# Optimization experiments

Hardware: AMD Instinct MI355X
Metric: run time of the kernel (lower is better)

Reference implementation:

```python
import jax, jax.numpy as jnp
import numpy as np

S, R, C, H, D = 128, 384, 256, 8, 32  # N_seq, N_res, C_m, heads, head_dim
INF = 1e9
EPS = 1e-5


def _layernorm(x, w, b):
    mu = jnp.mean(x, axis=-1, keepdims=True)
    var = jnp.mean(jnp.square(x - mu), axis=-1, keepdims=True)
    return (x - mu) * jax.lax.rsqrt(var + EPS) * w + b


def setup_inputs() -> dict:
    key = jax.random.key(0)
    ks = jax.random.split(key, 8)
    sc = 0.02
    m = jax.random.normal(ks[0], (S, R, C), jnp.float32)
    mask = jnp.ones((S, R), jnp.float32)
    ln_w = jnp.ones((C,), jnp.float32)
    ln_b = jnp.zeros((C,), jnp.float32)
    wq = jax.random.normal(ks[1], (C, H * D), jnp.float32) * sc
    wk = jax.random.normal(ks[2], (C, H * D), jnp.float32) * sc
    wv = jax.random.normal(ks[3], (C, H * D), jnp.float32) * sc
    wg = jax.random.normal(ks[4], (C, H * D), jnp.float32) * sc
    bg = jnp.ones((H * D,), jnp.float32)  # gate bias init to 1 (openfold convention)
    wo = jax.random.normal(ks[5], (H * D, C), jnp.float32) * sc
    bo = jnp.zeros((C,), jnp.float32)
    return {"m": m, "mask": mask, "ln_w": ln_w, "ln_b": ln_b,
            "wq": wq, "wk": wk, "wv": wv, "wg": wg, "bg": bg,
            "wo": wo, "bo": bo}


def reference(m, mask, ln_w, ln_b, wq, wk, wv, wg, bg, wo, bo):
    # mask bias: [S, 1, 1, R], 0 where mask==1, -inf-ish where mask==0
    mask_bias = (INF * (mask - 1.0))[:, None, None, :]
    x = _layernorm(m, ln_w, ln_b)                        # [S, R, C]
    q = (x @ wq).reshape(S, R, H, D) * (D ** -0.5)       # [S, R, H, D]
    k = (x @ wk).reshape(S, R, H, D)
    v = (x @ wv).reshape(S, R, H, D)
    scores = jnp.einsum('sqhd,skhd->shqk', q, k) + mask_bias  # [S, H, R, R]
    a = jax.nn.softmax(scores, axis=-1)
    o = jnp.einsum('shqk,skhd->sqhd', a, v)              # [S, R, H, D]
    g = jax.nn.sigmoid(x @ wg + bg).reshape(S, R, H, D)  # gate
    o = (o * g).reshape(S, R, H * D)
    return o @ wo + bo                                   # [S, R, C]
```

## Files before the change

### kernel.cpp

```cpp
#include <hip/hip_runtime.h>
#include <cstdint>
#include <cstddef>

#define S_  128
#define R_  384
#define C_  256
#define H_  8
#define D_  32
#define HD_ 256
#define M_  (S_*R_)

#define LOG2E 1.4426950408889634f

typedef float f32x16 __attribute__((ext_vector_type(16)));
typedef short s16x8  __attribute__((ext_vector_type(8)));
typedef int   i32x4  __attribute__((ext_vector_type(4)));

__device__ __forceinline__ unsigned short f2bf(float f) {
  uint32_t u = __float_as_uint(f);
  u += 0x7fffu + ((u >> 16) & 1u);
  return (unsigned short)(u >> 16);
}
__device__ __forceinline__ float bf2f(unsigned short s) {
  return __uint_as_float(((uint32_t)s) << 16);
}
__device__ __forceinline__ uint32_t pkbf(float lo, float hi) {
  return (uint32_t)f2bf(lo) | ((uint32_t)f2bf(hi) << 16);
}
#define MFMA32(a,b,c) __builtin_amdgcn_mfma_f32_32x32x16_bf16((a),(b),(c),0,0,0)

__device__ __forceinline__ void gload16(const void* g, void* l) {
  __builtin_amdgcn_global_load_lds(
      (const __attribute__((address_space(1))) void*)g,
      (__attribute__((address_space(3))) void*)l, 16, 0, 0);
}

__global__ __launch_bounds__(256) void prep_w(const float* __restrict__ wq,
    const float* __restrict__ wk, const float* __restrict__ wv,
    const float* __restrict__ wg, const float* __restrict__ wo,
    unsigned short* __restrict__ WT) {
  __shared__ unsigned short Tl[64][72];
  const int mat = blockIdx.x >> 4;
  const int t   = blockIdx.x & 15;
  const int k0  = (t >> 2) * 64, n0 = (t & 3) * 64;
  const float* W = (mat==0)?wq:(mat==1)?wk:(mat==2)?wv:(mat==3)?wg:wo;
  const int tx = threadIdx.x & 63, ty = threadIdx.x >> 6;
#pragma unroll
  for (int i = 0; i < 16; i++) {
    int kk = ty + i * 4;
    Tl[tx][kk] = f2bf(W[(size_t)(k0 + kk) * 256 + n0 + tx]);
  }
  __syncthreads();
#pragma unroll
  for (int i = 0; i < 16; i++) {
    int nn = ty + i * 4;
    WT[(size_t)mat * 65536 + (size_t)(n0 + nn) * 256 + k0 + tx] = Tl[nn][tx];
  }
}

__global__ __launch_bounds__(256) void ln_kernel(const float* __restrict__ mIn,
    const float* __restrict__ w, const float* __restrict__ b,
    unsigned short* __restrict__ x) {
  int row  = blockIdx.x * 4 + (threadIdx.x >> 6);
  int lane = threadIdx.x & 63;
  const float4 v4 = *(const float4*)(mIn + (size_t)row * C_ + lane * 4);
  float s  = v4.x + v4.y + v4.z + v4.w;
  float ss = v4.x*v4.x + v4.y*v4.y + v4.z*v4.z + v4.w*v4.w;
#pragma unroll
  for (int off = 32; off > 0; off >>= 1) {
    s  += __shfl_xor(s,  off);
    ss += __shfl_xor(ss, off);
  }
  float mu  = s * (1.0f / C_);
  float var = ss * (1.0f / C_) - mu * mu;
  float rs  = rsqrtf(var + 1e-5f);
  const float4 wv = *(const float4*)(w + lane * 4);
  const float4 bv = *(const float4*)(b + lane * 4);
  uint2 o2;
  o2.x = pkbf((v4.x - mu) * rs * wv.x + bv.x, (v4.y - mu) * rs * wv.y + bv.y);
  o2.y = pkbf((v4.z - mu) * rs * wv.z + bv.z, (v4.w - mu) * rs * wv.w + bv.w);
  *(uint2*)(x + (size_t)row * C_ + lane * 4) = o2;
}

__global__ __launch_bounds__(256) void proj_gemm(const unsigned short* __restrict__ X,
    const unsigned short* __restrict__ WT, const float* __restrict__ bg,
    unsigned short* __restrict__ Qo, unsigned short* __restrict__ Ko,
    unsigned short* __restrict__ Vo, unsigned short* __restrict__ Go) {
  __shared__ __align__(16) unsigned short As[128 * 32];
  __shared__ __align__(16) unsigned short Bs[128 * 32];
  const int tid = threadIdx.x;
  const int bm  = blockIdx.x * 128;
  const int wi  = blockIdx.y >> 1;
  const int bn  = (blockIdx.y & 1) * 128;
  const unsigned short* Wt = WT + (size_t)wi * 65536;
  unsigned short* O = (wi==0)?Qo:(wi==1)?Ko:(wi==2)?Vo:Go;

  const int lane = tid & 63, wid = tid >> 6;
  const int wm = (wid >> 1) * 64, wn = (wid & 1) * 64;
  const int lr = lane & 31, hi = lane >> 5;
  const int srow = lane >> 2, scol = (lane & 3) * 8;

  f32x16 acc[2][2];
#pragma unroll
  for (int i = 0; i < 2; i++)
#pragma unroll
    for (int j = 0; j < 2; j++)
#pragma unroll
      for (int r = 0; r < 16; r++) acc[i][j][r] = 0.f;

  for (int k0 = 0; k0 < 256; k0 += 32) {
#pragma unroll
    for (int i = 0; i < 2; i++) {
      const int rbase = wid * 32 + i * 16;
      gload16(X  + (size_t)(bm + rbase + srow) * 256 + k0 + scol, &As[rbase * 32]);
      gload16(Wt + (size_t)(bn + rbase + srow) * 256 + k0 + scol, &Bs[rbase * 32]);
    }
    asm volatile("s_waitcnt vmcnt(0)" ::: "memory");
    __syncthreads();
#pragma unroll
    for (int kh = 0; kh < 2; kh++) {
      s16x8 a0 = *(const s16x8*)&As[(wm + lr) * 32      + kh*16 + 8*hi];
      s16x8 a1 = *(const s16x8*)&As[(wm + 32 + lr) * 32 + kh*16 + 8*hi];
      s16x8 b0 = *(const s16x8*)&Bs[(wn + lr) * 32      + kh*16 + 8*hi];
      s16x8 b1 = *(const s16x8*)&Bs[(wn + 32 + lr) * 32 + kh*16 + 8*hi];
      acc[0][0] = MFMA32(a0, b0, acc[0][0]);
      acc[0][1] = MFMA32(a0, b1, acc[0][1]);
      acc[1][0] = MFMA32(a1, b0, acc[1][0]);
      acc[1][1] = MFMA32(a1, b1, acc[1][1]);
    }
    __syncthreads();
  }

  const float qs2 = 0.17677669529663687f * LOG2E;
#pragma unroll
  for (int ms = 0; ms < 2; ms++) {
#pragma unroll
    for (int ns = 0; ns < 2; ns++) {
      int colg = bn + wn + ns*32 + lr;
      float bgv = (wi == 3) ? bg[colg] : 0.f;
#pragma unroll
      for (int r = 0; r < 16; r++) {
        float v = acc[ms][ns][r];
        if (wi == 0) v *= qs2;
        if (wi == 3) v = 1.0f / (1.0f + __expf(-(v + bgv)));
        int row = bm + wm + ms*32 + (r & 3) + 8*(r >> 2) + 4*hi;
        O[(size_t)row * 256 + colg] = f2bf(v);
      }
    }
  }
}

__global__ __launch_bounds__(256) void attn_kernel(const unsigned short* __restrict__ Qb,
    const unsigned short* __restrict__ Kb, const unsigned short* __restrict__ Vb,
    const unsigned short* __restrict__ Gb, const float* __restrict__ mask,
    unsigned short* __restrict__ Ob) {
  __shared__ unsigned short Kl[192][40];
  __shared__ unsigned short VT[32][200];
  __shared__ float mb[384];
  __shared__ float sAl[4][32];

  const int h = blockIdx.x, s = blockIdx.y;
  const int tid = threadIdx.x;
  const int wid = tid >> 6;
  const int lane = tid & 63;
  const int lr = lane & 31, hi = lane >> 5;

  for (int r = tid; r < 384; r += 256)
    mb[r] = (1e9f * LOG2E) * (mask[s * R_ + r] - 1.0f);

  s16x8 bq[3][2];
#pragma unroll
  for (int st = 0; st < 3; st++)
#pragma unroll
    for (int kh = 0; kh < 2; kh++)
      bq[st][kh] = *(const s16x8*)(Qb + ((size_t)(s*R_ + wid*96 + st*32 + lr)) * 256
                                   + h*32 + kh*16 + 8*hi);

  f32x16 of[3];
#pragma unroll
  for (int st = 0; st < 3; st++)
#pragma unroll
    for (int r = 0; r < 16; r++) of[st][r] = 0.f;
  float mrun[3] = {-1e30f, -1e30f, -1e30f};
  float lsum[3] = {0.f, 0.f, 0.f};

  for (int ph = 0; ph < 2; ph++) {
    __syncthreads();
#pragma unroll
    for (int i = 0; i < 2; i++) {
      int rh = tid + 256 * i;
      if (rh < 384) {
        int rl = rh >> 1, c0 = (rh & 1) * 16;
        int rg = ph * 192 + rl;
        const unsigned short* ksrc = Kb + ((size_t)(s*R_ + rg)) * 256 + h*32 + c0;
        *(uint4*)&Kl[rl][c0]     = *(const uint4*)ksrc;
        *(uint4*)&Kl[rl][c0 + 8] = *(const uint4*)(ksrc + 8);
        const unsigned short* vsrc = Vb + ((size_t)(s*R_ + rg)) * 256 + h*32 + c0;
        unsigned short tmp[16];
        *(uint4*)tmp       = *(const uint4*)vsrc;
        *(uint4*)(tmp + 8) = *(const uint4*)(vsrc + 8);
#pragma unroll
        for (int j = 0; j < 16; j++) VT[c0 + j][rl] = tmp[j];
      }
    }
    __syncthreads();

    for (int kt = 0; kt < 6; kt++) {
      const int ktg = ph * 6 + kt;
      s16x8 ak0 = *(const s16x8*)&Kl[kt*32 + lr][8*hi];
      s16x8 ak1 = *(const s16x8*)&Kl[kt*32 + lr][16 + 8*hi];
      s16x8 bv0 = *(const s16x8*)&VT[lr][kt*32 + 8*hi];
      s16x8 bv1 = *(const s16x8*)&VT[lr][kt*32 + 16 + 8*hi];
      float mbr[16];
#pragma unroll
      for (int r = 0; r < 16; r++) mbr[r] = mb[ktg*32 + (r & 3) + 8*(r >> 2) + 4*hi];

#pragma unroll
      for (int st = 0; st < 3; st++) {
        f32x16 p;
#pragma unroll
        for (int r = 0; r < 16; r++) p[r] = mbr[r];
        __builtin_amdgcn_s_setprio(1);
        p = MFMA32(ak0, bq[st][0], p);
        p = MFMA32(ak1, bq[st][1], p);
        __builtin_amdgcn_s_setprio(0);
        float m01 = fmaxf(fmaxf(p[0], p[1]), fmaxf(p[2], p[3]));
        float m23 = fmaxf(fmaxf(p[4], p[5]), fmaxf(p[6], p[7]));
        float m45 = fmaxf(fmaxf(p[8], p[9]), fmaxf(p[10], p[11]));
        float m67 = fmaxf(fmaxf(p[12], p[13]), fmaxf(p[14], p[15]));
        float pm = fmaxf(fmaxf(m01, m23), fmaxf(m45, m67));
        pm = fmaxf(pm, __shfl_xor(pm, 32));
        if (!__all(pm <= mrun[st] + 11.54f)) {
          float nm = fmaxf(mrun[st], pm);
          float al = __builtin_amdgcn_exp2f(mrun[st] - nm);
          mrun[st] = nm;
          lsum[st] *= al;
          if (hi == 0) sAl[wid][lr] = al;
          float alr[16];
#pragma unroll
          for (int r = 0; r < 16; r++) alr[r] = sAl[wid][(r & 3) + 8*(r >> 2) + 4*hi];
#pragma unroll
          for (int r = 0; r < 16; r++) of[st][r] *= alr[r];
        }
        float ls = 0.f;
#pragma unroll
        for (int r = 0; r < 16; r++) {
          p[r] = __builtin_amdgcn_exp2f(p[r] - mrun[st]);
          ls += p[r];
        }
        lsum[st] += ls;
        uint32_t w0 = pkbf(p[0],  p[1]),  w1 = pkbf(p[2],  p[3]);
        uint32_t w2 = pkbf(p[4],  p[5]),  w3 = pkbf(p[6],  p[7]);
        uint32_t w4 = pkbf(p[8],  p[9]),  w5 = pkbf(p[10], p[11]);
        uint32_t w6 = pkbf(p[12], p[13]), w7 = pkbf(p[14], p[15]);
        asm volatile("v_permlane32_swap_b32 %0, %1" : "+v"(w0), "+v"(w2));
        asm volatile("v_permlane32_swap_b32 %0, %1" : "+v"(w1), "+v"(w3));
        asm volatile("v_permlane32_swap_b32 %0, %1" : "+v"(w4), "+v"(w6));
        asm volatile("v_permlane32_swap_b32 %0, %1" : "+v"(w5), "+v"(w7));
        i32x4 pa0i = {(int)w0, (int)w1, (int)w2, (int)w3};
        i32x4 pa1i = {(int)w4, (int)w5, (int)w6, (int)w7};
        __builtin_amdgcn_s_setprio(1);
        of[st] = MFMA32(__builtin_bit_cast(s16x8, pa0i), bv0, of[st]);
        of[st] = MFMA32(__builtin_bit_cast(s16x8, pa1i), bv1, of[st]);
        __builtin_amdgcn_s_setprio(0);
      }
    }
  }

#pragma unroll
  for (int st = 0; st < 3; st++) {
    float lt = lsum[st] + __shfl_xor(lsum[st], 32);
    float inv = 1.0f / lt;
    if (hi == 0) sAl[wid][lr] = inv;
    float ivr[16];
#pragma unroll
    for (int r = 0; r < 16; r++) ivr[r] = sAl[wid][(r & 3) + 8*(r >> 2) + 4*hi];
#pragma unroll
    for (int r = 0; r < 16; r++) {
      int row = wid*96 + st*32 + (r & 3) + 8*(r >> 2) + 4*hi;
      size_t off = ((size_t)(s*R_ + row)) * 256 + h*32 + lr;
      float gv = bf2f(Gb[off]);
      Ob[off] = f2bf(of[st][r] * ivr[r] * gv);
    }
  }
}

__global__ __launch_bounds__(256) void out_gemm(const unsigned short* __restrict__ Ob,
    const unsigned short* __restrict__ WT, const float* __restrict__ bo,
    float* __restrict__ Out) {
  __shared__ __align__(16) unsigned short As[128 * 32];
  __shared__ __align__(16) unsigned short Bs[128 * 32];
  const unsigned short* Wt = WT + 4 * 65536;
  const int tid = threadIdx.x;
  const int bm = blockIdx.x * 128;
  const int bn = blockIdx.y * 128;
  const int lane = tid & 63, wid = tid >> 6;
  const int wm = (wid >> 1) * 64, wn = (wid & 1) * 64;
  const int lr = lane & 31, hi = lane >> 5;
  const int srow = lane >> 2, scol = (lane & 3) * 8;

  f32x16 acc[2][2];
#pragma unroll
  for (int i = 0; i < 2; i++)
#pragma unroll
    for (int j = 0; j < 2; j++)
#pragma unroll
      for (int r = 0; r < 16; r++) acc[i][j][r] = 0.f;

  for (int k0 = 0; k0 < 256; k0 += 32) {
#pragma unroll
    for (int i = 0; i < 2; i++) {
      const int rbase = wid * 32 + i * 16;
      gload16(Ob + (size_t)(bm + rbase + srow) * 256 + k0 + scol, &As[rbase * 32]);
      gload16(Wt + (size_t)(bn + rbase + srow) * 256 + k0 + scol, &Bs[rbase * 32]);
    }
    asm volatile("s_waitcnt vmcnt(0)" ::: "memory");
    __syncthreads();
#pragma unroll
    for (int kh = 0; kh < 2; kh++) {
      s16x8 a0 = *(const s16x8*)&As[(wm + lr) * 32      + kh*16 + 8*hi];
      s16x8 a1 = *(const s16x8*)&As[(wm + 32 + lr) * 32 + kh*16 + 8*hi];
      s16x8 b0 = *(const s16x8*)&Bs[(wn + lr) * 32      + kh*16 + 8*hi];
      s16x8 b1 = *(const s16x8*)&Bs[(wn + 32 + lr) * 32 + kh*16 + 8*hi];
      acc[0][0] = MFMA32(a0, b0, acc[0][0]);
      acc[0][1] = MFMA32(a0, b1, acc[0][1]);
      acc[1][0] = MFMA32(a1, b0, acc[1][0]);
      acc[1][1] = MFMA32(a1, b1, acc[1][1]);
    }
    __syncthreads();
  }

#pragma unroll
  for (int ms = 0; ms < 2; ms++) {
#pragma unroll
    for (int ns = 0; ns < 2; ns++) {
      int colg = bn + wn + ns*32 + lr;
      float bov = bo[colg];
#pragma unroll
      for (int r = 0; r < 16; r++) {
        int row = bm + wm + ms*32 + (r & 3) + 8*(r >> 2) + 4*hi;
        Out[(size_t)row * 256 + colg] = acc[ms][ns][r] + bov;
      }
    }
  }
}

extern "C" void kernel_launch(void* const* d_in, const int* in_sizes, int n_in,
                              void* d_out, int out_size, void* d_ws, size_t ws_size,
                              hipStream_t stream) {
  const float* m    = (const float*)d_in[0];
  const float* mask = (const float*)d_in[1];
  const float* ln_w = (const float*)d_in[2];
  const float* ln_b = (const float*)d_in[3];
  const float* wq   = (const float*)d_in[4];
  const float* wk   = (const float*)d_in[5];
  const float* wv   = (const float*)d_in[6];
  const float* wg   = (const float*)d_in[7];
  const float* bg   = (const float*)d_in[8];
  const float* wo   = (const float*)d_in[9];
  const float* bo   = (const float*)d_in[10];
  float* out = (float*)d_out;

  unsigned short* ws = (unsigned short*)d_ws;
  const size_t SZ = (size_t)M_ * 256;
  unsigned short* xbf = ws;
  unsigned short* qb  = ws + 1 * SZ;
  unsigned short* kb  = ws + 2 * SZ;
  unsigned short* vb  = ws + 3 * SZ;
  unsigned short* gb  = ws + 4 * SZ;
  unsigned short* ob  = ws + 5 * SZ;
  unsigned short* WT  = ws + 6 * SZ;

  prep_w<<<80, 256, 0, stream>>>(wq, wk, wv, wg, wo, WT);
  ln_kernel<<<M_ / 4, 256, 0, stream>>>(m, ln_w, ln_b, xbf);
  proj_gemm<<<dim3(M_ / 128, 8), 256, 0, stream>>>(xbf, WT, bg, qb, kb, vb, gb);
  attn_kernel<<<dim3(H_, S_), 256, 0, stream>>>(qb, kb, vb, gb, mask, ob);
  out_gemm<<<dim3(M_ / 128, 2), 256, 0, stream>>>(ob, WT, bo, out);
}
```

Measured before the change: 262.3 us.

## Shrink GEMM tiles, reorder grids, and use 12-wave attention blocks

```diff
diff --git a/kernel.cpp b/kernel.cpp
--- a/kernel.cpp
+++ b/kernel.cpp
@@ -82,265 +82,233 @@
   *(uint2*)(x + (size_t)row * C_ + lane * 4) = o2;
 }
 
-__global__ __launch_bounds__(256) void proj_gemm(const unsigned short* __restrict__ X,
+__global__ __launch_bounds__(256, 5) void proj_gemm(const unsigned short* __restrict__ X,
     const unsigned short* __restrict__ WT, const float* __restrict__ bg,
     unsigned short* __restrict__ Qo, unsigned short* __restrict__ Ko,
     unsigned short* __restrict__ Vo, unsigned short* __restrict__ Go) {
-  __shared__ __align__(16) unsigned short As[128 * 32];
+  __shared__ __align__(16) unsigned short As[64 * 32];
   __shared__ __align__(16) unsigned short Bs[128 * 32];
   const int tid = threadIdx.x;
-  const int bm  = blockIdx.x * 128;
-  const int wi  = blockIdx.y >> 1;
-  const int bn  = (blockIdx.y & 1) * 128;
+  const int wi  = blockIdx.x >> 1;
+  const int bn  = (blockIdx.x & 1) * 128;
+  const int bm  = blockIdx.y * 64;
   const unsigned short* Wt = WT + (size_t)wi * 65536;
   unsigned short* O = (wi==0)?Qo:(wi==1)?Ko:(wi==2)?Vo:Go;
 
   const int lane = tid & 63, wid = tid >> 6;
-  const int wm = (wid >> 1) * 64, wn = (wid & 1) * 64;
+  const int wr = (wid >> 1) * 32, wc = (wid & 1) * 64;
   const int lr = lane & 31, hi = lane >> 5;
   const int srow = lane >> 2, scol = (lane & 3) * 8;
 
-  f32x16 acc[2][2];
-#pragma unroll
-  for (int i = 0; i < 2; i++)
-#pragma unroll
-    for (int j = 0; j < 2; j++)
-#pragma unroll
-      for (int r = 0; r < 16; r++) acc[i][j][r] = 0.f;
+  f32x16 acc0, acc1;
+#pragma unroll
+  for (int r = 0; r < 16; r++) { acc0[r] = 0.f; acc1[r] = 0.f; }
 
   for (int k0 = 0; k0 < 256; k0 += 32) {
+    gload16(X + (size_t)(bm + wid*16 + srow) * 256 + k0 + scol, &As[wid * 512]);
 #pragma unroll
     for (int i = 0; i < 2; i++) {
-      const int rbase = wid * 32 + i * 16;
-      gload16(X  + (size_t)(bm + rbase + srow) * 256 + k0 + scol, &As[rbase * 32]);
-      gload16(Wt + (size_t)(bn + rbase + srow) * 256 + k0 + scol, &Bs[rbase * 32]);
+      const int rb = wid * 32 + i * 16;
+      gload16(Wt + (size_t)(bn + rb + srow) * 256 + k0 + scol, &Bs[rb * 32]);
     }
     asm volatile("s_waitcnt vmcnt(0)" ::: "memory");
     __syncthreads();
 #pragma unroll
     for (int kh = 0; kh < 2; kh++) {
-      s16x8 a0 = *(const s16x8*)&As[(wm + lr) * 32      + kh*16 + 8*hi];
-      s16x8 a1 = *(const s16x8*)&As[(wm + 32 + lr) * 32 + kh*16 + 8*hi];
-      s16x8 b0 = *(const s16x8*)&Bs[(wn + lr) * 32      + kh*16 + 8*hi];
-      s16x8 b1 = *(const s16x8*)&Bs[(wn + 32 + lr) * 32 + kh*16 + 8*hi];
-      acc[0][0] = MFMA32(a0, b0, acc[0][0]);
-      acc[0][1] = MFMA32(a0, b1, acc[0][1]);
-      acc[1][0] = MFMA32(a1, b0, acc[1][0]);
-      acc[1][1] = MFMA32(a1, b1, acc[1][1]);
+      s16x8 a0 = *(const s16x8*)&As[(wr + lr) * 32      + kh*16 + 8*hi];
+      s16x8 b0 = *(const s16x8*)&Bs[(wc + lr) * 32      + kh*16 + 8*hi];
+      s16x8 b1 = *(const s16x8*)&Bs[(wc + 32 + lr) * 32 + kh*16 + 8*hi];
+      acc0 = MFMA32(a0, b0, acc0);
+      acc1 = MFMA32(a0, b1, acc1);
     }
     __syncthreads();
   }
 
   const float qs2 = 0.17677669529663687f * LOG2E;
 #pragma unroll
-  for (int ms = 0; ms < 2; ms++) {
-#pragma unroll
-    for (int ns = 0; ns < 2; ns++) {
-      int colg = bn + wn + ns*32 + lr;
-      float bgv = (wi == 3) ? bg[colg] : 0.f;
-#pragma unroll
-      for (int r = 0; r < 16; r++) {
-        float v = acc[ms][ns][r];
-        if (wi == 0) v *= qs2;
-        if (wi == 3) v = 1.0f / (1.0f + __expf(-(v + bgv)));
-        int row = bm + wm + ms*32 + (r & 3) + 8*(r >> 2) + 4*hi;
-        O[(size_t)row * 256 + colg] = f2bf(v);
-      }
-    }
-  }
-}
-
-__global__ __launch_bounds__(256) void attn_kernel(const unsigned short* __restrict__ Qb,
+  for (int ns = 0; ns < 2; ns++) {
+    const f32x16& a = ns ? acc1 : acc0;
+    int colg = bn + wc + ns*32 + lr;
+    float bgv = (wi == 3) ? bg[colg] : 0.f;
+#pragma unroll
+    for (int r = 0; r < 16; r++) {
+      float v = a[r];
+      if (wi == 0) v *= qs2;
+      if (wi == 3) v = 1.0f / (1.0f + __expf(-(v + bgv)));
+      int row = bm + wr + (r & 3) + 8*(r >> 2) + 4*hi;
+      O[(size_t)row * 256 + colg] = f2bf(v);
+    }
+  }
+}
+
+__global__ __launch_bounds__(768, 6) void attn_kernel(const unsigned short* __restrict__ Qb,
     const unsigned short* __restrict__ Kb, const unsigned short* __restrict__ Vb,
     const unsigned short* __restrict__ Gb, const float* __restrict__ mask,
     unsigned short* __restrict__ Ob) {
-  __shared__ unsigned short Kl[192][40];
-  __shared__ unsigned short VT[32][200];
+  __shared__ unsigned short Kl[384][40];
+  __shared__ unsigned short VT[32][392];
   __shared__ float mb[384];
-  __shared__ float sAl[4][32];
+  __shared__ float sAl[12][32];
 
   const int h = blockIdx.x, s = blockIdx.y;
   const int tid = threadIdx.x;
-  const int wid = tid >> 6;
-  const int lane = tid & 63;
+  const int wid = tid >> 6, lane = tid & 63;
   const int lr = lane & 31, hi = lane >> 5;
 
-  for (int r = tid; r < 384; r += 256)
-    mb[r] = (1e9f * LOG2E) * (mask[s * R_ + r] - 1.0f);
-
-  s16x8 bq[3][2];
-#pragma unroll
-  for (int st = 0; st < 3; st++)
-#pragma unroll
-    for (int kh = 0; kh < 2; kh++)
-      bq[st][kh] = *(const s16x8*)(Qb + ((size_t)(s*R_ + wid*96 + st*32 + lr)) * 256
-                                   + h*32 + kh*16 + 8*hi);
-
-  f32x16 of[3];
-#pragma unroll
-  for (int st = 0; st < 3; st++)
-#pragma unroll
-    for (int r = 0; r < 16; r++) of[st][r] = 0.f;
-  float mrun[3] = {-1e30f, -1e30f, -1e30f};
-  float lsum[3] = {0.f, 0.f, 0.f};
-
-  for (int ph = 0; ph < 2; ph++) {
-    __syncthreads();
-#pragma unroll
-    for (int i = 0; i < 2; i++) {
-      int rh = tid + 256 * i;
-      if (rh < 384) {
-        int rl = rh >> 1, c0 = (rh & 1) * 16;
-        int rg = ph * 192 + rl;
-        const unsigned short* ksrc = Kb + ((size_t)(s*R_ + rg)) * 256 + h*32 + c0;
-        *(uint4*)&Kl[rl][c0]     = *(const uint4*)ksrc;
-        *(uint4*)&Kl[rl][c0 + 8] = *(const uint4*)(ksrc + 8);
-        const unsigned short* vsrc = Vb + ((size_t)(s*R_ + rg)) * 256 + h*32 + c0;
-        unsigned short tmp[16];
-        *(uint4*)tmp       = *(const uint4*)vsrc;
-        *(uint4*)(tmp + 8) = *(const uint4*)(vsrc + 8);
-#pragma unroll
-        for (int j = 0; j < 16; j++) VT[c0 + j][rl] = tmp[j];
-      }
-    }
-    __syncthreads();
-
-    for (int kt = 0; kt < 6; kt++) {
-      const int ktg = ph * 6 + kt;
-      s16x8 ak0 = *(const s16x8*)&Kl[kt*32 + lr][8*hi];
-      s16x8 ak1 = *(const s16x8*)&Kl[kt*32 + lr][16 + 8*hi];
-      s16x8 bv0 = *(const s16x8*)&VT[lr][kt*32 + 8*hi];
-      s16x8 bv1 = *(const s16x8*)&VT[lr][kt*32 + 16 + 8*hi];
-      float mbr[16];
-#pragma unroll
-      for (int r = 0; r < 16; r++) mbr[r] = mb[ktg*32 + (r & 3) + 8*(r >> 2) + 4*hi];
-
-#pragma unroll
-      for (int st = 0; st < 3; st++) {
-        f32x16 p;
-#pragma unroll
-        for (int r = 0; r < 16; r++) p[r] = mbr[r];
-        __builtin_amdgcn_s_setprio(1);
-        p = MFMA32(ak0, bq[st][0], p);
-        p = MFMA32(ak1, bq[st][1], p);
-        __builtin_amdgcn_s_setprio(0);
-        float m01 = fmaxf(fmaxf(p[0], p[1]), fmaxf(p[2], p[3]));
-        float m23 = fmaxf(fmaxf(p[4], p[5]), fmaxf(p[6], p[7]));
-        float m45 = fmaxf(fmaxf(p[8], p[9]), fmaxf(p[10], p[11]));
-        float m67 = fmaxf(fmaxf(p[12], p[13]), fmaxf(p[14], p[15]));
-        float pm = fmaxf(fmaxf(m01, m23), fmaxf(m45, m67));
-        pm = fmaxf(pm, __shfl_xor(pm, 32));
-        if (!__all(pm <= mrun[st] + 11.54f)) {
-          float nm = fmaxf(mrun[st], pm);
-          float al = __builtin_amdgcn_exp2f(mrun[st] - nm);
-          mrun[st] = nm;
-          lsum[st] *= al;
-          if (hi == 0) sAl[wid][lr] = al;
-          float alr[16];
-#pragma unroll
-          for (int r = 0; r < 16; r++) alr[r] = sAl[wid][(r & 3) + 8*(r >> 2) + 4*hi];
-#pragma unroll
-          for (int r = 0; r < 16; r++) of[st][r] *= alr[r];
-        }
-        float ls = 0.f;
-#pragma unroll
-        for (int r = 0; r < 16; r++) {
-          p[r] = __builtin_amdgcn_exp2f(p[r] - mrun[st]);
-          ls += p[r];
-        }
-        lsum[st] += ls;
-        uint32_t w0 = pkbf(p[0],  p[1]),  w1 = pkbf(p[2],  p[3]);
-        uint32_t w2 = pkbf(p[4],  p[5]),  w3 = pkbf(p[6],  p[7]);
-        uint32_t w4 = pkbf(p[8],  p[9]),  w5 = pkbf(p[10], p[11]);
-        uint32_t w6 = pkbf(p[12], p[13]), w7 = pkbf(p[14], p[15]);
-        asm volatile("v_permlane32_swap_b32 %0, %1" : "+v"(w0), "+v"(w2));
-        asm volatile("v_permlane32_swap_b32 %0, %1" : "+v"(w1), "+v"(w3));
-        asm volatile("v_permlane32_swap_b32 %0, %1" : "+v"(w4), "+v"(w6));
-        asm volatile("v_permlane32_swap_b32 %0, %1" : "+v"(w5), "+v"(w7));
-        i32x4 pa0i = {(int)w0, (int)w1, (int)w2, (int)w3};
-        i32x4 pa1i = {(int)w4, (int)w5, (int)w6, (int)w7};
-        __builtin_amdgcn_s_setprio(1);
-        of[st] = MFMA32(__builtin_bit_cast(s16x8, pa0i), bv0, of[st]);
-        of[st] = MFMA32(__builtin_bit_cast(s16x8, pa1i), bv1, of[st]);
-        __builtin_amdgcn_s_setprio(0);
-      }
-    }
-  }
-
-#pragma unroll
-  for (int st = 0; st < 3; st++) {
-    float lt = lsum[st] + __shfl_xor(lsum[st], 32);
-    float inv = 1.0f / lt;
-    if (hi == 0) sAl[wid][lr] = inv;
-    float ivr[16];
-#pragma unroll
-    for (int r = 0; r < 16; r++) ivr[r] = sAl[wid][(r & 3) + 8*(r >> 2) + 4*hi];
+  if (tid < 384) {
+    const unsigned short* ksrc = Kb + ((size_t)(s*R_ + tid)) * 256 + h*32;
+    uint4 k0 = *(const uint4*)ksrc;
+    uint4 k1 = *(const uint4*)(ksrc + 8);
+    uint4 k2 = *(const uint4*)(ksrc + 16);
+    uint4 k3 = *(const uint4*)(ksrc + 24);
+    *(uint4*)&Kl[tid][0]  = k0;
+    *(uint4*)&Kl[tid][8]  = k1;
+    *(uint4*)&Kl[tid][16] = k2;
+    *(uint4*)&Kl[tid][24] = k3;
+    mb[tid] = (1e9f * LOG2E) * (mask[s * R_ + tid] - 1.0f);
+  } else {
+    const int r = tid - 384;
+    const unsigned short* vsrc = Vb + ((size_t)(s*R_ + r)) * 256 + h*32;
+    unsigned short tmp[32];
+    *(uint4*)(tmp)      = *(const uint4*)vsrc;
+    *(uint4*)(tmp + 8)  = *(const uint4*)(vsrc + 8);
+    *(uint4*)(tmp + 16) = *(const uint4*)(vsrc + 16);
+    *(uint4*)(tmp + 24) = *(const uint4*)(vsrc + 24);
+#pragma unroll
+    for (int j = 0; j < 32; j++) VT[j][r] = tmp[j];
+  }
+
+  const int q0 = wid * 32;
+  const unsigned short* qsrc = Qb + ((size_t)(s*R_ + q0 + lr)) * 256 + h*32;
+  s16x8 bq0 = *(const s16x8*)(qsrc + 8*hi);
+  s16x8 bq1 = *(const s16x8*)(qsrc + 16 + 8*hi);
+
+  f32x16 of;
+#pragma unroll
+  for (int r = 0; r < 16; r++) of[r] = 0.f;
+  float mrun = -1e30f, lsum = 0.f;
+
+  __syncthreads();
+
+  for (int kt = 0; kt < 12; kt++) {
+    s16x8 ak0 = *(const s16x8*)&Kl[kt*32 + lr][8*hi];
+    s16x8 ak1 = *(const s16x8*)&Kl[kt*32 + lr][16 + 8*hi];
+    s16x8 bv0 = *(const s16x8*)&VT[lr][kt*32 + 8*hi];
+    s16x8 bv1 = *(const s16x8*)&VT[lr][kt*32 + 16 + 8*hi];
+
+    f32x16 p;
+#pragma unroll
+    for (int r = 0; r < 16; r++) p[r] = mb[kt*32 + (r & 3) + 8*(r >> 2) + 4*hi];
+    __builtin_amdgcn_s_setprio(1);
+    p = MFMA32(ak0, bq0, p);
+    p = MFMA32(ak1, bq1, p);
+    __builtin_amdgcn_s_setprio(0);
+
+    float m01 = fmaxf(fmaxf(p[0], p[1]), fmaxf(p[2], p[3]));
+    float m23 = fmaxf(fmaxf(p[4], p[5]), fmaxf(p[6], p[7]));
+    float m45 = fmaxf(fmaxf(p[8], p[9]), fmaxf(p[10], p[11]));
+    float m67 = fmaxf(fmaxf(p[12], p[13]), fmaxf(p[14], p[15]));
+    float pm = fmaxf(fmaxf(m01, m23), fmaxf(m45, m67));
+    pm = fmaxf(pm, __shfl_xor(pm, 32));
+    if (!__all(pm <= mrun + 11.54f)) {
+      float nm = fmaxf(mrun, pm);
+      float al = __builtin_amdgcn_exp2f(mrun - nm);
+      mrun = nm;
+      lsum *= al;
+      if (hi == 0) sAl[wid][lr] = al;
+#pragma unroll
+      for (int r = 0; r < 16; r++)
+        of[r] *= sAl[wid][(r & 3) + 8*(r >> 2) + 4*hi];
+    }
+    float ls = 0.f;
 #pragma unroll
     for (int r = 0; r < 16; r++) {
-      int row = wid*96 + st*32 + (r & 3) + 8*(r >> 2) + 4*hi;
-      size_t off = ((size_t)(s*R_ + row)) * 256 + h*32 + lr;
-      float gv = bf2f(Gb[off]);
-      Ob[off] = f2bf(of[st][r] * ivr[r] * gv);
-    }
-  }
-}
-
-__global__ __launch_bounds__(256) void out_gemm(const unsigned short* __restrict__ Ob,
+      p[r] = __builtin_amdgcn_exp2f(p[r] - mrun);
+      ls += p[r];
+    }
+    lsum += ls;
+
+    uint32_t w0, w1, w2, w3, w4, w5, w6, w7;
+    asm("v_cvt_pk_bf16_f32 %0, %1, %2" : "=v"(w0) : "v"(p[0]),  "v"(p[1]));
+    asm("v_cvt_pk_bf16_f32 %0, %1, %2" : "=v"(w1) : "v"(p[2]),  "v"(p[3]));
+    asm("v_cvt_pk_bf16_f32 %0, %1, %2" : "=v"(w2) : "v"(p[4]),  "v"(p[5]));
+    asm("v_cvt_pk_bf16_f32 %0, %1, %2" : "=v"(w3) : "v"(p[6]),  "v"(p[7]));
+    asm("v_cvt_pk_bf16_f32 %0, %1, %2" : "=v"(w4) : "v"(p[8]),  "v"(p[9]));
+    asm("v_cvt_pk_bf16_f32 %0, %1, %2" : "=v"(w5) : "v"(p[10]), "v"(p[11]));
+    asm("v_cvt_pk_bf16_f32 %0, %1, %2" : "=v"(w6) : "v"(p[12]), "v"(p[13]));
+    asm("v_cvt_pk_bf16_f32 %0, %1, %2" : "=v"(w7) : "v"(p[14]), "v"(p[15]));
+    asm volatile("v_permlane32_swap_b32 %0, %1" : "+v"(w0), "+v"(w2));
+    asm volatile("v_permlane32_swap_b32 %0, %1" : "+v"(w1), "+v"(w3));
+    asm volatile("v_permlane32_swap_b32 %0, %1" : "+v"(w4), "+v"(w6));
+    asm volatile("v_permlane32_swap_b32 %0, %1" : "+v"(w5), "+v"(w7));
+    i32x4 pa0i = {(int)w0, (int)w1, (int)w2, (int)w3};
+    i32x4 pa1i = {(int)w4, (int)w5, (int)w6, (int)w7};
+    __builtin_amdgcn_s_setprio(1);
+    of = MFMA32(__builtin_bit_cast(s16x8, pa0i), bv0, of);
+    of = MFMA32(__builtin_bit_cast(s16x8, pa1i), bv1, of);
+    __builtin_amdgcn_s_setprio(0);
+  }
+
+  float lt = lsum + __shfl_xor(lsum, 32);
+  float inv = 1.0f / lt;
+  if (hi == 0) sAl[wid][lr] = inv;
+#pragma unroll
+  for (int r = 0; r < 16; r++) {
+    int crow = (r & 3) + 8*(r >> 2) + 4*hi;
+    float iv = sAl[wid][crow];
+    size_t off = ((size_t)(s*R_ + q0 + crow)) * 256 + h*32 + lr;
+    float gv = bf2f(Gb[off]);
+    Ob[off] = f2bf(of[r] * iv * gv);
+  }
+}
+
+__global__ __launch_bounds__(256, 5) void out_gemm(const unsigned short* __restrict__ Ob,
     const unsigned short* __restrict__ WT, const float* __restrict__ bo,
     float* __restrict__ Out) {
-  __shared__ __align__(16) unsigned short As[128 * 32];
+  __shared__ __align__(16) unsigned short As[64 * 32];
   __shared__ __align__(16) unsigned short Bs[128 * 32];
   const unsigned short* Wt = WT + 4 * 65536;
   const int tid = threadIdx.x;
-  const int bm = blockIdx.x * 128;
-  const int bn = blockIdx.y * 128;
+  const int bn = blockIdx.x * 128;
+  const int bm = blockIdx.y * 64;
   const int lane = tid & 63, wid = tid >> 6;
-  const int wm = (wid >> 1) * 64, wn = (wid & 1) * 64;
+  const int wr = (wid >> 1) * 32, wc = (wid & 1) * 64;
   const int lr = lane & 31, hi = lane >> 5;
   const int srow = lane >> 2, scol = (lane & 3) * 8;
 
-  f32x16 acc[2][2];
-#pragma unroll
-  for (int i = 0; i < 2; i++)
-#pragma unroll
-    for (int j = 0; j < 2; j++)
-#pragma unroll
-      for (int r = 0; r < 16; r++) acc[i][j][r] = 0.f;
+  f32x16 acc0, acc1;
+#pragma unroll
+  for (int r = 0; r < 16; r++) { acc0[r] = 0.f; acc1[r] = 0.f; }
 
   for (int k0 = 0; k0 < 256; k0 += 32) {
+    gload16(Ob + (size_t)(bm + wid*16 + srow) * 256 + k0 + scol, &As[wid * 512]);
 #pragma unroll
     for (int i = 0; i < 2; i++) {
-      const int rbase = wid * 32 + i * 16;
-      gload16(Ob + (size_t)(bm + rbase + srow) * 256 + k0 + scol, &As[rbase * 32]);
-      gload16(Wt + (size_t)(bn + rbase + srow) * 256 + k0 + scol, &Bs[rbase * 32]);
+      const int rb = wid * 32 + i * 16;
+      gload16(Wt + (size_t)(bn + rb + srow) * 256 + k0 + scol, &Bs[rb * 32]);
     }
     asm volatile("s_waitcnt vmcnt(0)" ::: "memory");
     __syncthreads();
 #pragma unroll
     for (int kh = 0; kh < 2; kh++) {
-      s16x8 a0 = *(const s16x8*)&As[(wm + lr) * 32      + kh*16 + 8*hi];
-      s16x8 a1 = *(const s16x8*)&As[(wm + 32 + lr) * 32 + kh*16 + 8*hi];
-      s16x8 b0 = *(const s16x8*)&Bs[(wn + lr) * 32      + kh*16 + 8*hi];
-      s16x8 b1 = *(const s16x8*)&Bs[(wn + 32 + lr) * 32 + kh*16 + 8*hi];
-      acc[0][0] = MFMA32(a0, b0, acc[0][0]);
-      acc[0][1] = MFMA32(a0, b1, acc[0][1]);
-      acc[1][0] = MFMA32(a1, b0, acc[1][0]);
-      acc[1][1] = MFMA32(a1, b1, acc[1][1]);
+      s16x8 a0 = *(const s16x8*)&As[(wr + lr) * 32      + kh*16 + 8*hi];
+      s16x8 b0 = *(const s16x8*)&Bs[(wc + lr) * 32      + kh*16 + 8*hi];
+      s16x8 b1 = *(const s16x8*)&Bs[(wc + 32 + lr) * 32 + kh*16 + 8*hi];
+      acc0 = MFMA32(a0, b0, acc0);
+      acc1 = MFMA32(a0, b1, acc1);
     }
     __syncthreads();
   }
 
 #pragma unroll
-  for (int ms = 0; ms < 2; ms++) {
-#pragma unroll
-    for (int ns = 0; ns < 2; ns++) {
-      int colg = bn + wn + ns*32 + lr;
-      float bov = bo[colg];
-#pragma unroll
-      for (int r = 0; r < 16; r++) {
-        int row = bm + wm + ms*32 + (r & 3) + 8*(r >> 2) + 4*hi;
-        Out[(size_t)row * 256 + colg] = acc[ms][ns][r] + bov;
-      }
+  for (int ns = 0; ns < 2; ns++) {
+    const f32x16& a = ns ? acc1 : acc0;
+    int colg = bn + wc + ns*32 + lr;
+    float bov = bo[colg];
+#pragma unroll
+    for (int r = 0; r < 16; r++) {
+      int row = bm + wr + (r & 3) + 8*(r >> 2) + 4*hi;
+      Out[(size_t)row * 256 + colg] = a[r] + bov;
     }
   }
 }
@@ -373,7 +341,7 @@
 
   prep_w<<<80, 256, 0, stream>>>(wq, wk, wv, wg, wo, WT);
   ln_kernel<<<M_ / 4, 256, 0, stream>>>(m, ln_w, ln_b, xbf);
-  proj_gemm<<<dim3(M_ / 128, 8), 256, 0, stream>>>(xbf, WT, bg, qb, kb, vb, gb);
-  attn_kernel<<<dim3(H_, S_), 256, 0, stream>>>(qb, kb, vb, gb, mask, ob);
-  out_gemm<<<dim3(M_ / 128, 2), 256, 0, stream>>>(ob, WT, bo, out);
-}
+  proj_gemm<<<dim3(8, M_ / 64), 256, 0, stream>>>(xbf, WT, bg, qb, kb, vb, gb);
+  attn_kernel<<<dim3(H_, S_), 768, 0, stream>>>(qb, kb, vb, gb, mask, ob);
+  out_gemm<<<dim3(2, M_ / 64), 256, 0, stream>>>(ob, WT, bo, out);
+}
```

Result: faster. 241.4 us (-8.0%).
